# Optimization experiments

Measured on AMD Instinct MI355X. Metric: run time of the kernel, lower is better.

Reference implementation:

```python
import jax, jax.numpy as jnp
import numpy as np

D_MODEL = 1024
N_HEADS = 16
D_K = D_MODEL // N_HEADS
D_FF = 4096
B, S = 2, 2048
EPS = 1e-5
SCALE = 0.02


def setup_inputs() -> dict:
    key = jax.random.key(0)
    ks = jax.random.split(key, 8)
    return {
        "x": jax.random.normal(ks[0], (B, S, D_MODEL), dtype=jnp.float32),
        "ln1_w": jnp.ones((D_MODEL,), jnp.float32),
        "ln1_b": jnp.zeros((D_MODEL,), jnp.float32),
        "Wq": jax.random.normal(ks[1], (D_MODEL, D_MODEL), jnp.float32) * SCALE,
        "bq": jnp.zeros((D_MODEL,), jnp.float32),
        "Wk": jax.random.normal(ks[2], (D_MODEL, D_MODEL), jnp.float32) * SCALE,
        "bk": jnp.zeros((D_MODEL,), jnp.float32),
        "Wv": jax.random.normal(ks[3], (D_MODEL, D_MODEL), jnp.float32) * SCALE,
        "bv": jnp.zeros((D_MODEL,), jnp.float32),
        "Wo": jax.random.normal(ks[4], (D_MODEL, D_MODEL), jnp.float32) * SCALE,
        "bo": jnp.zeros((D_MODEL,), jnp.float32),
        "ln2_w": jnp.ones((D_MODEL,), jnp.float32),
        "ln2_b": jnp.zeros((D_MODEL,), jnp.float32),
        "W1": jax.random.normal(ks[5], (D_MODEL, D_FF), jnp.float32) * SCALE,
        "b1": jnp.zeros((D_FF,), jnp.float32),
        "W2": jax.random.normal(ks[6], (D_FF, D_MODEL), jnp.float32) * SCALE,
        "b2": jnp.zeros((D_MODEL,), jnp.float32),
    }


def _layernorm(x, w, b):
    mu = jnp.mean(x, axis=-1, keepdims=True)
    var = jnp.mean(jnp.square(x - mu), axis=-1, keepdims=True)
    return (x - mu) * jax.lax.rsqrt(var + EPS) * w + b


def reference(x, ln1_w, ln1_b, Wq, bq, Wk, bk, Wv, bv, Wo, bo,
              ln2_w, ln2_b, W1, b1, W2, b2):
    # Pre-norm multi-head self-attention (dropout = identity, eval mode)
    h = _layernorm(x, ln1_w, ln1_b)                      # [B,S,D]
    q = (h @ Wq + bq).reshape(B, S, N_HEADS, D_K)        # [B,S,H,Dk]
    k = (h @ Wk + bk).reshape(B, S, N_HEADS, D_K)
    v = (h @ Wv + bv).reshape(B, S, N_HEADS, D_K)
    scores = jnp.einsum('bqhd,bkhd->bhqk', q, k) / jnp.sqrt(jnp.float32(D_K))
    attn = jax.nn.softmax(scores, axis=-1)               # [B,H,S,S]
    ctx = jnp.einsum('bhqk,bkhd->bqhd', attn, v).reshape(B, S, D_MODEL)
    x = x + (ctx @ Wo + bo)
    # Pre-norm FFN
    h2 = _layernorm(x, ln2_w, ln2_b)
    ff = jax.nn.relu(h2 @ W1 + b1) @ W2 + b2
    return x + ff
```

## Files before the change

### kernel.cpp

```cpp
#include <hip/hip_runtime.h>
#include <hip/hip_bf16.h>
#include <cstdint>
#include <cstddef>

typedef unsigned short ushort_t;
typedef __bf16 bf16x8 __attribute__((ext_vector_type(8)));
typedef float f32x4 __attribute__((ext_vector_type(4)));
typedef float f32x16 __attribute__((ext_vector_type(16)));

#define D_MODEL 1024
#define D_FF 4096
#define BB 2
#define SS 2048
#define NH 16
#define MROWS (BB * SS)
#define KVBLK 64

__device__ __forceinline__ ushort_t f2bf(float f) {
  union { float f; unsigned u; } x; x.f = f;
  unsigned r = x.u + 0x7fffu + ((x.u >> 16) & 1u);
  return (ushort_t)(r >> 16);
}

__device__ __forceinline__ void gload_lds16(const void* g, void* l) {
  __builtin_amdgcn_global_load_lds((const __attribute__((address_space(1))) void*)g,
                                   (__attribute__((address_space(3))) void*)l, 16, 0, 0);
}

__device__ __forceinline__ bf16x8 pack4w(unsigned w0, unsigned w1, unsigned w2, unsigned w3) {
  union { unsigned u[4]; bf16x8 v; } t;
  t.u[0] = w0; t.u[1] = w1; t.u[2] = w2; t.u[3] = w3;
  return t.v;
}

__global__ __launch_bounds__(256) void ln_bf16_kernel(
    const float* __restrict__ x, const float* __restrict__ w,
    const float* __restrict__ b, ushort_t* __restrict__ out) {
  int row = blockIdx.x;
  int tid = threadIdx.x;
  int lane = tid & 63, wid = tid >> 6;
  const float4 v = ((const float4*)(x + (size_t)row * D_MODEL))[tid];
  float s = v.x + v.y + v.z + v.w;
  __shared__ float red[8];
  #pragma unroll
  for (int o = 32; o > 0; o >>= 1) s += __shfl_down(s, o);
  if (lane == 0) red[wid] = s;
  __syncthreads();
  float mu = (red[0] + red[1] + red[2] + red[3]) * (1.0f / D_MODEL);
  float d0 = v.x - mu, d1 = v.y - mu, d2 = v.z - mu, d3 = v.w - mu;
  float sq = d0 * d0 + d1 * d1 + d2 * d2 + d3 * d3;
  #pragma unroll
  for (int o = 32; o > 0; o >>= 1) sq += __shfl_down(sq, o);
  if (lane == 0) red[4 + wid] = sq;
  __syncthreads();
  float var = (red[4] + red[5] + red[6] + red[7]) * (1.0f / D_MODEL);
  float rstd = rsqrtf(var + 1e-5f);
  const float4 wv = ((const float4*)w)[tid];
  const float4 bv = ((const float4*)b)[tid];
  ushort4 o4;
  o4.x = f2bf(d0 * rstd * wv.x + bv.x);
  o4.y = f2bf(d1 * rstd * wv.y + bv.y);
  o4.z = f2bf(d2 * rstd * wv.z + bv.z);
  o4.w = f2bf(d3 * rstd * wv.w + bv.w);
  ((ushort4*)(out + (size_t)row * D_MODEL))[tid] = o4;
}

__global__ __launch_bounds__(256) void transpose_cast_kernel(
    const float* __restrict__ W, ushort_t* __restrict__ Wt, int K, int N) {
  __shared__ float tile[32][33];
  int bx = blockIdx.x * 32;
  int by = blockIdx.y * 32;
  int tx = threadIdx.x, ty = threadIdx.y;
  #pragma unroll
  for (int i = 0; i < 32; i += 8)
    tile[ty + i][tx] = W[(size_t)(by + ty + i) * N + bx + tx];
  __syncthreads();
  #pragma unroll
  for (int i = 0; i < 32; i += 8)
    Wt[(size_t)(bx + ty + i) * K + by + tx] = f2bf(tile[tx][ty + i]);
}

__global__ __launch_bounds__(256) void transpose_cast4_kernel(
    const float* __restrict__ Wq, const float* __restrict__ Wk,
    const float* __restrict__ Wv, const float* __restrict__ Wo,
    ushort_t* __restrict__ Dqkv, ushort_t* __restrict__ Do_) {
  __shared__ float tile[32][33];
  int z = blockIdx.z;
  const float* W = (z == 0) ? Wq : (z == 1) ? Wk : (z == 2) ? Wv : Wo;
  ushort_t* Wt = (z < 3) ? (Dqkv + (size_t)z * 1024 * 1024) : Do_;
  int bx = blockIdx.x * 32;
  int by = blockIdx.y * 32;
  int tx = threadIdx.x, ty = threadIdx.y;
  #pragma unroll
  for (int i = 0; i < 32; i += 8)
    tile[ty + i][tx] = W[(size_t)(by + ty + i) * 1024 + bx + tx];
  __syncthreads();
  #pragma unroll
  for (int i = 0; i < 32; i += 8)
    Wt[(size_t)(bx + ty + i) * 1024 + by + tx] = f2bf(tile[tx][ty + i]);
}

__global__ __launch_bounds__(256) void biaspack_kernel(
    const float* __restrict__ bq, const float* __restrict__ bk,
    const float* __restrict__ bv, float* __restrict__ out) {
  int i = blockIdx.x * 256 + threadIdx.x;
  float v = (i < 1024) ? bq[i] : (i < 2048) ? bk[i - 1024] : bv[i - 2048];
  out[i] = v;
}

__global__ __launch_bounds__(256) void vtrans_kernel(
    const ushort_t* __restrict__ qkv, ushort_t* __restrict__ Vt) {
  __shared__ __align__(16) ushort_t T[64 * 64];
  const int tid = threadIdx.x;
  const int bh = blockIdx.y, b = bh >> 4, h = bh & 15;
  const int kv0 = blockIdx.x * 64;
  const ushort_t* Vp = qkv + (size_t)b * SS * 3072 + 2048 + h * 64;
  #pragma unroll
  for (int i = 0; i < 2; i++) {
    int idx = tid * 2 + i;
    int key = idx >> 3, c = idx & 7;
    bf16x8 v = *(const bf16x8*)(Vp + (size_t)(kv0 + key) * 3072 + c * 8);
    *(bf16x8*)(T + key * 64 + ((c ^ (key & 7)) * 8)) = v;
  }
  __syncthreads();
  int d = tid >> 2, kb = tid & 3;
  ushort_t o[16];
  #pragma unroll
  for (int j = 0; j < 16; j++) {
    int key = kb * 16 + j;
    o[j] = T[key * 64 + (((d >> 3) ^ (key & 7)) * 8) + (d & 7)];
  }
  ushort_t* dst = Vt + (size_t)(bh * 64 + d) * SS + kv0 + kb * 16;
  *(bf16x8*)dst = *(bf16x8*)&o[0];
  *(bf16x8*)(dst + 8) = *(bf16x8*)&o[8];
}

template <int EPI>
__global__ __launch_bounds__(256, 2) void gemm256w_kernel(
    const ushort_t* __restrict__ A, const ushort_t* __restrict__ Bt,
    const float* __restrict__ bias, void* __restrict__ Cout,
    int M, int N, int K, int NTn) {
  __shared__ __align__(16) ushort_t ldsA[3][4096];
  __shared__ __align__(16) ushort_t ldsB[3][8192];
  const int tid = threadIdx.x, lane = tid & 63, wid = tid >> 6;
  const int wm = wid >> 1, wn = wid & 1;
  const int rl = lane & 15, cg = lane >> 4;
  int nwg = gridDim.x;
  int q = nwg >> 3, rr = nwg & 7;
  int xcd = blockIdx.x & 7, idx = blockIdx.x >> 3;
  int wgid = (xcd < rr ? xcd * (q + 1) : rr * (q + 1) + (xcd - rr) * q) + idx;
  const int row0 = (wgid / NTn) * 128, col0 = (wgid - (wgid / NTn) * NTn) * 256;
  const int NT = K / 32;

  int soffA[2], ldsoA[2], soffB[4], ldsoB[4];
  #pragma unroll
  for (int i = 0; i < 2; i++) {
    int ci = wid * 128 + i * 64 + lane;
    int P = ci * 16;
    int L = P ^ (((P >> 7) & 7) << 4);
    soffA[i] = (L >> 6) * K + ((L >> 4) & 3) * 8;
    ldsoA[i] = (wid * 128 + i * 64) * 8;
  }
  #pragma unroll
  for (int i = 0; i < 4; i++) {
    int ci = wid * 256 + i * 64 + lane;
    int P = ci * 16;
    int L = P ^ (((P >> 7) & 7) << 4);
    soffB[i] = (L >> 6) * K + ((L >> 4) & 3) * 8;
    ldsoB[i] = (wid * 256 + i * 64) * 8;
  }

  f32x4 acc[4][8] = {};

  auto stage = [&](int t, int b) {
    int kk = t * 32;
    #pragma unroll
    for (int i = 0; i < 2; i++)
      gload_lds16(A + (size_t)row0 * K + kk + soffA[i], &ldsA[b][ldsoA[i]]);
    #pragma unroll
    for (int i = 0; i < 4; i++)
      gload_lds16(Bt + (size_t)col0 * K + kk + soffB[i], &ldsB[b][ldsoB[i]]);
  };

  auto compute = [&](int b) {
    bf16x8 af[4], bfv[8];
    #pragma unroll
    for (int mi = 0; mi < 4; mi++) {
      int r = wm * 64 + mi * 16 + rl;
      int L = r * 64 + cg * 16;
      int P = L ^ (((L >> 7) & 7) << 4);
      af[mi] = *(const bf16x8*)&ldsA[b][P >> 1];
    }
    #pragma unroll
    for (int ni = 0; ni < 8; ni++) {
      int r = wn * 128 + ni * 16 + rl;
      int L = r * 64 + cg * 16;
      int P = L ^ (((L >> 7) & 7) << 4);
      bfv[ni] = *(const bf16x8*)&ldsB[b][P >> 1];
    }
    __builtin_amdgcn_s_setprio(1);
    #pragma unroll
    for (int mi = 0; mi < 4; mi++)
      #pragma unroll
      for (int ni = 0; ni < 8; ni++)
        acc[mi][ni] = __builtin_amdgcn_mfma_f32_16x16x32_bf16(af[mi], bfv[ni], acc[mi][ni], 0, 0, 0);
    __builtin_amdgcn_s_setprio(0);
  };

  stage(0, 0); stage(1, 1);
  int sb = 2, cb = 0;
  for (int t = 0; t < NT; ++t) {
    if (t < NT - 1) asm volatile("s_waitcnt vmcnt(6)" ::: "memory");
    else            asm volatile("s_waitcnt vmcnt(0)" ::: "memory");
    __builtin_amdgcn_s_barrier();
    __builtin_amdgcn_sched_barrier(0);
    if (t + 2 < NT) { stage(t + 2, sb); sb = (sb == 2) ? 0 : sb + 1; }
    compute(cb);
    cb = (cb == 2) ? 0 : cb + 1;
  }

  ushort_t* out = (ushort_t*)Cout;
  #pragma unroll
  for (int ni = 0; ni < 8; ni++) {
    int col = col0 + wn * 128 + ni * 16 + rl;
    float bv = bias[col];
    float sc = (EPI == 0 && col < 1024) ? 0.18033688011f : 1.0f;
    #pragma unroll
    for (int mi = 0; mi < 4; mi++) {
      int rowb = row0 + wm * 64 + mi * 16 + cg * 4;
      #pragma unroll
      for (int j = 0; j < 4; j++) {
        float v = acc[mi][ni][j] + bv;
        if (EPI == 1) v = fmaxf(v, 0.0f);
        if (EPI == 0) v *= sc;
        out[(size_t)(rowb + j) * N + col] = f2bf(v);
      }
    }
  }
}

template <int EPI>
__global__ __launch_bounds__(256, 3) void gemm128_kernel(
    const ushort_t* __restrict__ A, const ushort_t* __restrict__ Bt,
    const float* __restrict__ bias, const float* __restrict__ resid,
    void* __restrict__ Cout, int M, int N, int K, int NTn, int Ksplit, int MTN) {
  __shared__ __align__(16) ushort_t lds[3][2][4096];
  const int tid = threadIdx.x, lane = tid & 63, wid = tid >> 6;
  const int wm = wid >> 1, wn = wid & 1;
  const int rl = lane & 15, cg = lane >> 4;
  int nwg = gridDim.x;
  int q = nwg >> 3, rr = nwg & 7;
  int xcd = blockIdx.x & 7, idx = blockIdx.x >> 3;
  int wgid = (xcd < rr ? xcd * (q + 1) : rr * (q + 1) + (xcd - rr) * q) + idx;
  const int s = wgid / MTN;
  int rem = wgid - s * MTN;
  const int row0 = (rem / NTn) * 128, col0 = (rem - (rem / NTn) * NTn) * 128;
  const int k0 = s * Ksplit;
  const int NT = Ksplit / 32;

  int soff[2], ldso[2];
  #pragma unroll
  for (int i = 0; i < 2; i++) {
    int ci = wid * 128 + i * 64 + lane;
    int P = ci * 16;
    int L = P ^ (((P >> 7) & 7) << 4);
    int row = L >> 6, kc = (L >> 4) & 3;
    soff[i] = row * K + kc * 8;
    ldso[i] = (wid * 128 + i * 64) * 8;
  }

  f32x4 acc[4][4] = {};

  auto stage = [&](int t, int b) {
    int kk = k0 + t * 32;
    #pragma unroll
    for (int i = 0; i < 2; i++) {
      gload_lds16(A + (size_t)row0 * K + kk + soff[i], &lds[b][0][ldso[i]]);
      gload_lds16(Bt + (size_t)col0 * K + kk + soff[i], &lds[b][1][ldso[i]]);
    }
  };

  auto compute = [&](int b) {
    bf16x8 af[4], bfv[4];
    #pragma unroll
    for (int mi = 0; mi < 4; mi++) {
      int r = wm * 64 + mi * 16 + rl;
      int L = r * 64 + cg * 16;
      int P = L ^ (((L >> 7) & 7) << 4);
      af[mi] = *(const bf16x8*)&lds[b][0][P >> 1];
    }
    #pragma unroll
    for (int ni = 0; ni < 4; ni++) {
      int r = wn * 64 + ni * 16 + rl;
      int L = r * 64 + cg * 16;
      int P = L ^ (((L >> 7) & 7) << 4);
      bfv[ni] = *(const bf16x8*)&lds[b][1][P >> 1];
    }
    __builtin_amdgcn_s_setprio(1);
    #pragma unroll
    for (int mi = 0; mi < 4; mi++)
      #pragma unroll
      for (int ni = 0; ni < 4; ni++)
        acc[mi][ni] = __builtin_amdgcn_mfma_f32_16x16x32_bf16(af[mi], bfv[ni], acc[mi][ni], 0, 0, 0);
    __builtin_amdgcn_s_setprio(0);
  };

  stage(0, 0); stage(1, 1);
  int sb = 2, cb = 0;
  for (int t = 0; t < NT; ++t) {
    if (t < NT - 1) asm volatile("s_waitcnt vmcnt(4)" ::: "memory");
    else            asm volatile("s_waitcnt vmcnt(0)" ::: "memory");
    __builtin_amdgcn_s_barrier();
    __builtin_amdgcn_sched_barrier(0);
    if (t + 2 < NT) { stage(t + 2, sb); sb = (sb == 2) ? 0 : sb + 1; }
    compute(cb);
    cb = (cb == 2) ? 0 : cb + 1;
  }

  if (EPI == 2) {
    float* out = (float*)Cout;
    #pragma unroll
    for (int ni = 0; ni < 4; ni++) {
      int col = col0 + wn * 64 + ni * 16 + rl;
      float bv = bias[col];
      #pragma unroll
      for (int mi = 0; mi < 4; mi++) {
        int rowb = row0 + wm * 64 + mi * 16 + cg * 4;
        #pragma unroll
        for (int j = 0; j < 4; j++)
          out[(size_t)(rowb + j) * N + col] =
              acc[mi][ni][j] + bv + resid[(size_t)(rowb + j) * N + col];
      }
    }
  } else {
    float* out = (float*)Cout + (size_t)s * M * N;
    #pragma unroll
    for (int ni = 0; ni < 4; ni++) {
      int col = col0 + wn * 64 + ni * 16 + rl;
      #pragma unroll
      for (int mi = 0; mi < 4; mi++) {
        int rowb = row0 + wm * 64 + mi * 16 + cg * 4;
        #pragma unroll
        for (int j = 0; j < 4; j++)
          out[(size_t)(rowb + j) * N + col] = acc[mi][ni][j];
      }
    }
  }
}

__global__ __launch_bounds__(256) void reduce_kernel(
    const float* __restrict__ p, const float* __restrict__ bias,
    const float* __restrict__ resid, float* __restrict__ out,
    int S, size_t total4, size_t stride4) {
  const float4* p4 = (const float4*)p;
  const float4* r4 = (const float4*)resid;
  const float4* b4 = (const float4*)bias;
  float4* o4 = (float4*)out;
  for (size_t i = (size_t)blockIdx.x * 256 + threadIdx.x; i < total4;
       i += (size_t)gridDim.x * 256) {
    float4 a = r4[i];
    float4 bb = b4[i & 255];
    a.x += bb.x; a.y += bb.y; a.z += bb.z; a.w += bb.w;
    for (int s = 0; s < S; ++s) {
      float4 v = p4[(size_t)s * stride4 + i];
      a.x += v.x; a.y += v.y; a.z += v.z; a.w += v.w;
    }
    o4[i] = a;
  }
}

__global__ __launch_bounds__(256) void attn_kernel(
    const ushort_t* __restrict__ qkv, const ushort_t* __restrict__ Vt,
    ushort_t* __restrict__ ctx) {
  __shared__ __align__(16) ushort_t Kl[2][64 * 64];
  __shared__ __align__(16) ushort_t Vl[2][64 * 64];
  __shared__ float Lt[4][32];
  const int tid = threadIdx.x, lane = tid & 63, wid = tid >> 6;
  int bid = blockIdx.y * 16 + blockIdx.x;
  int w = (bid & 7) * 64 + (bid >> 3);
  const int bh = w >> 4, qt = w & 15;
  const int b = bh >> 4, h = bh & 15;
  const int q0w = qt * 128 + wid * 32;
  const int k31 = lane & 31, sg = lane >> 5, x7 = k31 & 7;
  const ushort_t* Qp = qkv + (size_t)b * SS * 3072 + h * 64;
  const ushort_t* Kp = Qp + 1024;
  const ushort_t* Vg = Vt + (size_t)bh * 64 * SS;

  bf16x8 qf[4];
  {
    const ushort_t* qb = Qp + (size_t)(q0w + k31) * 3072 + sg * 8;
    #pragma unroll
    for (int dsl = 0; dsl < 4; dsl++)
      qf[dsl] = *(const bf16x8*)(qb + dsl * 16);
  }
  float lsum = 0.f;
  f32x16 o0 = {}, o1 = {};

  const int NT = SS / KVBLK;

  int ksrc[2], vsrc[2];
  #pragma unroll
  for (int i = 0; i < 2; i++) {
    int idx = wid * 128 + i * 64 + lane;
    int R = idx >> 3, c = idx & 7;
    ksrc[i] = R * 3072 + ((c ^ (R & 7)) * 8);
    vsrc[i] = R * SS + ((c ^ (R & 7)) * 8);
  }
  const int ldsb = wid * 1024;

  auto stageKV = [&](int buf, int t) {
    size_t kvK = (size_t)t * KVBLK * 3072;
    int kvV = t * KVBLK;
    gload_lds16(Kp + kvK + ksrc[0], &Kl[buf][ldsb]);
    gload_lds16(Kp + kvK + ksrc[1], &Kl[buf][ldsb + 512]);
    gload_lds16(Vg + kvV + vsrc[0], &Vl[buf][ldsb]);
    gload_lds16(Vg + kvV + vsrc[1], &Vl[buf][ldsb + 512]);
  };

  auto softmax_half = [&](const f32x16& s, bf16x8& paE, bf16x8& paO) {
    float pv[16];
    #pragma unroll
    for (int r = 0; r < 16; r++) pv[r] = __builtin_amdgcn_exp2f(s[r]);
    #pragma unroll
    for (int r = 0; r < 16; r++) lsum += pv[r];
    unsigned W[4][2];
    #pragma unroll
    for (int qd = 0; qd < 4; qd++) {
      asm("v_cvt_pk_bf16_f32 %0, %1, %2" : "=v"(W[qd][0]) : "v"(pv[4 * qd]), "v"(pv[4 * qd + 1]));
      asm("v_cvt_pk_bf16_f32 %0, %1, %2" : "=v"(W[qd][1]) : "v"(pv[4 * qd + 2]), "v"(pv[4 * qd + 3]));
    }
    unsigned a0 = W[1][0], b0 = W[0][0], a1 = W[1][1], b1 = W[0][1];
    asm("v_permlane32_swap_b32 %0, %1" : "+v"(a0), "+v"(b0));
    asm("v_permlane32_swap_b32 %0, %1" : "+v"(a1), "+v"(b1));
    paE = pack4w(b0, b1, a0, a1);
    unsigned a2 = W[3][0], b2 = W[2][0], a3 = W[3][1], b3 = W[2][1];
    asm("v_permlane32_swap_b32 %0, %1" : "+v"(a2), "+v"(b2));
    asm("v_permlane32_swap_b32 %0, %1" : "+v"(a3), "+v"(b3));
    paO = pack4w(b2, b3, a2, a3);
  };

  auto body = [&](int t, int cb) {
    __syncthreads();
    if (t + 1 < NT) stageKV(cb ^ 1, t + 1);

    f32x16 s0 = {}, s1 = {};
    #pragma unroll
    for (int dsl = 0; dsl < 4; dsl++) {
      int ch = ((dsl * 2 + sg) ^ x7) * 8;
      bf16x8 kf0 = *(const bf16x8*)(&Kl[cb][k31 * 64 + ch]);
      bf16x8 kf1 = *(const bf16x8*)(&Kl[cb][(32 + k31) * 64 + ch]);
      s0 = __builtin_amdgcn_mfma_f32_32x32x16_bf16(kf0, qf[dsl], s0, 0, 0, 0);
      s1 = __builtin_amdgcn_mfma_f32_32x32x16_bf16(kf1, qf[dsl], s1, 0, 0, 0);
    }
    bf16x8 pa[4];
    softmax_half(s0, pa[0], pa[1]);
    softmax_half(s1, pa[2], pa[3]);
    #pragma unroll
    for (int ks = 0; ks < 4; ks++) {
      int ch = ((2 * ks + sg) ^ x7) * 8;
      bf16x8 vf0 = *(const bf16x8*)(&Vl[cb][k31 * 64 + ch]);
      bf16x8 vf1 = *(const bf16x8*)(&Vl[cb][(32 + k31) * 64 + ch]);
      o0 = __builtin_amdgcn_mfma_f32_32x32x16_bf16(pa[ks], vf0, o0, 0, 0, 0);
      o1 = __builtin_amdgcn_mfma_f32_32x32x16_bf16(pa[ks], vf1, o1, 0, 0, 0);
    }
  };

  stageKV(0, 0);
  for (int t = 0; t < NT; t += 2) {
    body(t, 0);
    body(t + 1, 1);
  }

  float ltot = lsum + __shfl_xor(lsum, 32);
  if (lane < 32) Lt[wid][lane] = ltot;
  asm volatile("s_waitcnt lgkmcnt(0)" ::: "memory");
  __builtin_amdgcn_sched_barrier(0);

  const int colb = h * 64 + k31;
  #pragma unroll
  for (int r = 0; r < 16; r++) {
    int qp = (r & 3) + 8 * (r >> 2) + 4 * sg;
    float rlq = 1.0f / Lt[wid][qp];
    size_t row = (size_t)(b * SS + q0w + qp);
    ctx[row * D_MODEL + colb] = f2bf(o0[r] * rlq);
    ctx[row * D_MODEL + colb + 32] = f2bf(o1[r] * rlq);
  }
}

extern "C" void kernel_launch(void* const* d_in, const int* in_sizes, int n_in,
                              void* d_out, int out_size, void* d_ws, size_t ws_size,
                              hipStream_t stream) {
  const float* x    = (const float*)d_in[0];
  const float* ln1w = (const float*)d_in[1];
  const float* ln1b = (const float*)d_in[2];
  const float* Wq   = (const float*)d_in[3];
  const float* bq   = (const float*)d_in[4];
  const float* Wk   = (const float*)d_in[5];
  const float* bk   = (const float*)d_in[6];
  const float* Wv   = (const float*)d_in[7];
  const float* bv   = (const float*)d_in[8];
  const float* Wo   = (const float*)d_in[9];
  const float* bo   = (const float*)d_in[10];
  const float* ln2w = (const float*)d_in[11];
  const float* ln2b = (const float*)d_in[12];
  const float* W1   = (const float*)d_in[13];
  const float* b1   = (const float*)d_in[14];
  const float* W2   = (const float*)d_in[15];
  const float* b2   = (const float*)d_in[16];

  char* ws = (char*)d_ws;
  size_t off = 0;
  auto alloc = [&](size_t bytes) {
    void* p = ws + off;
    off += (bytes + 255) & ~(size_t)255;
    return p;
  };
  ushort_t* Wt_qkv = (ushort_t*)alloc((size_t)3072 * 1024 * 2);
  ushort_t* Wt_o   = (ushort_t*)alloc((size_t)1024 * 1024 * 2);
  ushort_t* Wt_1   = (ushort_t*)alloc((size_t)4096 * 1024 * 2);
  ushort_t* Wt_2   = (ushort_t*)alloc((size_t)1024 * 4096 * 2);
  float*    bqkv   = (float*)alloc((size_t)3072 * 4);
  ushort_t* qkvb   = (ushort_t*)alloc((size_t)MROWS * 3072 * 2);
  ushort_t* ctxb   = (ushort_t*)alloc((size_t)MROWS * 1024 * 2);
  ushort_t* hbuf   = (ushort_t*)alloc((size_t)MROWS * 1024 * 2);
  float*    x2     = (float*)alloc((size_t)MROWS * 1024 * 4);
  ushort_t* Vtb    = (ushort_t*)alloc((size_t)BB * NH * 64 * SS * 2);
  ushort_t* ff1    = qkvb;
  float*    outp   = (float*)d_out;

  const size_t partial1 = (size_t)MROWS * 1024 * 4;
  int S = (ws_size - off >= 2 * partial1 + 256) ? 2 : 1;
  float* pbuf = (S == 2) ? (float*)alloc(2 * partial1) : nullptr;

  dim3 tb(32, 8);
  transpose_cast4_kernel<<<dim3(32, 32, 4), tb, 0, stream>>>(Wq, Wk, Wv, Wo, Wt_qkv, Wt_o);
  transpose_cast_kernel<<<dim3(128, 32), tb, 0, stream>>>(W1, Wt_1, 1024, 4096);
  transpose_cast_kernel<<<dim3(32, 128), tb, 0, stream>>>(W2, Wt_2, 4096, 1024);
  biaspack_kernel<<<12, 256, 0, stream>>>(bq, bk, bv, bqkv);

  ln_bf16_kernel<<<MROWS, 256, 0, stream>>>(x, ln1w, ln1b, hbuf);
  gemm256w_kernel<0><<<dim3(32 * 12), 256, 0, stream>>>(
      hbuf, Wt_qkv, bqkv, qkvb, MROWS, 3072, 1024, 12);
  vtrans_kernel<<<dim3(SS / 64, BB * NH), 256, 0, stream>>>(qkvb, Vtb);
  attn_kernel<<<dim3(SS / 128, BB * NH), 256, 0, stream>>>(qkvb, Vtb, ctxb);
  gemm128_kernel<2><<<dim3(8 * 32), 256, 0, stream>>>(
      ctxb, Wt_o, bo, x, x2, MROWS, 1024, 1024, 8, 1024, 8 * 32);
  ln_bf16_kernel<<<MROWS, 256, 0, stream>>>(x2, ln2w, ln2b, hbuf);
  gemm256w_kernel<1><<<dim3(32 * 16), 256, 0, stream>>>(
      hbuf, Wt_1, b1, ff1, MROWS, D_FF, 1024, 16);
  if (S == 2) {
    gemm128_kernel<3><<<dim3(8 * 32 * 2), 256, 0, stream>>>(
        ff1, Wt_2, nullptr, nullptr, pbuf, MROWS, 1024, 4096, 8, 2048, 8 * 32);
    reduce_kernel<<<2048, 256, 0, stream>>>(pbuf, b2, x2, outp, 2,
        (size_t)MROWS * 1024 / 4, (size_t)MROWS * 1024 / 4);
  } else {
    gemm128_kernel<2><<<dim3(8 * 32), 256, 0, stream>>>(
        ff1, Wt_2, b2, x2, outp, MROWS, 1024, 4096, 8, 4096, 8 * 32);
  }
}
```

Before: 232.2 us.

## Triple-buffer attention K/V tiles with explicit vmcnt waits and split accumulators

The attention kernel moves from double- to triple-buffered K/V LDS tiles. It prefetches two tiles ahead and uses explicit s_waitcnt vmcnt plus a raw s_barrier instead of __syncthreads, so global loads stay in flight across iterations. The PV accumulators are split into four chains to shorten MFMA dependency chains, and the row-sum reduction becomes a tree. The cost is more LDS, which may lower occupancy, and extra accumulator registers.

```diff
diff --git a/kernel.cpp b/kernel.cpp
--- a/kernel.cpp
+++ b/kernel.cpp
@@ -372,8 +372,8 @@
 __global__ __launch_bounds__(256) void attn_kernel(
     const ushort_t* __restrict__ qkv, const ushort_t* __restrict__ Vt,
     ushort_t* __restrict__ ctx) {
-  __shared__ __align__(16) ushort_t Kl[2][64 * 64];
-  __shared__ __align__(16) ushort_t Vl[2][64 * 64];
+  __shared__ __align__(16) ushort_t Kl[3][64 * 64];
+  __shared__ __align__(16) ushort_t Vl[3][64 * 64];
   __shared__ float Lt[4][32];
   const int tid = threadIdx.x, lane = tid & 63, wid = tid >> 6;
   int bid = blockIdx.y * 16 + blockIdx.x;
@@ -394,7 +394,7 @@
       qf[dsl] = *(const bf16x8*)(qb + dsl * 16);
   }
   float lsum = 0.f;
-  f32x16 o0 = {}, o1 = {};
+  f32x16 oA = {}, oB = {}, oC = {}, oD = {};
 
   const int NT = SS / KVBLK;
 
@@ -421,28 +421,27 @@
     float pv[16];
     #pragma unroll
     for (int r = 0; r < 16; r++) pv[r] = __builtin_amdgcn_exp2f(s[r]);
-    #pragma unroll
-    for (int r = 0; r < 16; r++) lsum += pv[r];
+    float a0 = pv[0] + pv[1], a1 = pv[2] + pv[3], a2 = pv[4] + pv[5], a3 = pv[6] + pv[7];
+    float a4 = pv[8] + pv[9], a5 = pv[10] + pv[11], a6 = pv[12] + pv[13], a7 = pv[14] + pv[15];
+    float b0 = a0 + a1, b1 = a2 + a3, b2 = a4 + a5, b3 = a6 + a7;
+    lsum += (b0 + b1) + (b2 + b3);
     unsigned W[4][2];
     #pragma unroll
     for (int qd = 0; qd < 4; qd++) {
       asm("v_cvt_pk_bf16_f32 %0, %1, %2" : "=v"(W[qd][0]) : "v"(pv[4 * qd]), "v"(pv[4 * qd + 1]));
       asm("v_cvt_pk_bf16_f32 %0, %1, %2" : "=v"(W[qd][1]) : "v"(pv[4 * qd + 2]), "v"(pv[4 * qd + 3]));
     }
-    unsigned a0 = W[1][0], b0 = W[0][0], a1 = W[1][1], b1 = W[0][1];
-    asm("v_permlane32_swap_b32 %0, %1" : "+v"(a0), "+v"(b0));
-    asm("v_permlane32_swap_b32 %0, %1" : "+v"(a1), "+v"(b1));
-    paE = pack4w(b0, b1, a0, a1);
-    unsigned a2 = W[3][0], b2 = W[2][0], a3 = W[3][1], b3 = W[2][1];
-    asm("v_permlane32_swap_b32 %0, %1" : "+v"(a2), "+v"(b2));
-    asm("v_permlane32_swap_b32 %0, %1" : "+v"(a3), "+v"(b3));
-    paO = pack4w(b2, b3, a2, a3);
+    unsigned a0w = W[1][0], b0w = W[0][0], a1w = W[1][1], b1w = W[0][1];
+    asm("v_permlane32_swap_b32 %0, %1" : "+v"(a0w), "+v"(b0w));
+    asm("v_permlane32_swap_b32 %0, %1" : "+v"(a1w), "+v"(b1w));
+    paE = pack4w(b0w, b1w, a0w, a1w);
+    unsigned a2w = W[3][0], b2w = W[2][0], a3w = W[3][1], b3w = W[2][1];
+    asm("v_permlane32_swap_b32 %0, %1" : "+v"(a2w), "+v"(b2w));
+    asm("v_permlane32_swap_b32 %0, %1" : "+v"(a3w), "+v"(b3w));
+    paO = pack4w(b2w, b3w, a2w, a3w);
   };
 
   auto body = [&](int t, int cb) {
-    __syncthreads();
-    if (t + 1 < NT) stageKV(cb ^ 1, t + 1);
-
     f32x16 s0 = {}, s1 = {};
     #pragma unroll
     for (int dsl = 0; dsl < 4; dsl++) {
@@ -460,15 +459,27 @@
       int ch = ((2 * ks + sg) ^ x7) * 8;
       bf16x8 vf0 = *(const bf16x8*)(&Vl[cb][k31 * 64 + ch]);
       bf16x8 vf1 = *(const bf16x8*)(&Vl[cb][(32 + k31) * 64 + ch]);
-      o0 = __builtin_amdgcn_mfma_f32_32x32x16_bf16(pa[ks], vf0, o0, 0, 0, 0);
-      o1 = __builtin_amdgcn_mfma_f32_32x32x16_bf16(pa[ks], vf1, o1, 0, 0, 0);
+      if (ks < 2) {
+        oA = __builtin_amdgcn_mfma_f32_32x32x16_bf16(pa[ks], vf0, oA, 0, 0, 0);
+        oC = __builtin_amdgcn_mfma_f32_32x32x16_bf16(pa[ks], vf1, oC, 0, 0, 0);
+      } else {
+        oB = __builtin_amdgcn_mfma_f32_32x32x16_bf16(pa[ks], vf0, oB, 0, 0, 0);
+        oD = __builtin_amdgcn_mfma_f32_32x32x16_bf16(pa[ks], vf1, oD, 0, 0, 0);
+      }
     }
   };
 
   stageKV(0, 0);
-  for (int t = 0; t < NT; t += 2) {
-    body(t, 0);
-    body(t + 1, 1);
+  stageKV(1, 1);
+  int sb = 2, cb = 0;
+  for (int t = 0; t < NT; ++t) {
+    if (t < NT - 1) asm volatile("s_waitcnt vmcnt(4)" ::: "memory");
+    else            asm volatile("s_waitcnt vmcnt(0)" ::: "memory");
+    __builtin_amdgcn_s_barrier();
+    __builtin_amdgcn_sched_barrier(0);
+    if (t + 2 < NT) { stageKV(sb, t + 2); sb = (sb == 2) ? 0 : sb + 1; }
+    body(t, cb);
+    cb = (cb == 2) ? 0 : cb + 1;
   }
 
   float ltot = lsum + __shfl_xor(lsum, 32);
@@ -476,6 +487,7 @@
   asm volatile("s_waitcnt lgkmcnt(0)" ::: "memory");
   __builtin_amdgcn_sched_barrier(0);
 
+  f32x16 o0 = oA + oB, o1 = oC + oD;
   const int colb = h * 64 + k31;
   #pragma unroll
   for (int r = 0; r < 16; r++) {
```

After: 238.1 us. 1.03x slower.

## Split attention over two KV halves and combine partial outputs in a new kernel

Applied to the files above, without the earlier changes.

The attention kernel now runs a third grid dimension of two splits, each processing half of the key/value sequence. Each split writes unnormalised fp32 partial outputs and row sums to workspace. A new combine kernel adds the two halves, normalises and casts to bf16. The goal is to double the number of blocks so more CUs are busy, at the cost of extra fp32 global traffic and one more launch. Combining by simply adding the sums is only valid if the softmax applies no per-split running max. The FFN2 split-K path is also made unconditional by always allocating the partial buffer.

```diff
diff --git a/kernel.cpp b/kernel.cpp
--- a/kernel.cpp
+++ b/kernel.cpp
@@ -371,11 +371,11 @@
 
 __global__ __launch_bounds__(256) void attn_kernel(
     const ushort_t* __restrict__ qkv, const ushort_t* __restrict__ Vt,
-    ushort_t* __restrict__ ctx) {
+    float* __restrict__ Op, float* __restrict__ Lp) {
   __shared__ __align__(16) ushort_t Kl[2][64 * 64];
   __shared__ __align__(16) ushort_t Vl[2][64 * 64];
-  __shared__ float Lt[4][32];
   const int tid = threadIdx.x, lane = tid & 63, wid = tid >> 6;
+  const int split = blockIdx.z;
   int bid = blockIdx.y * 16 + blockIdx.x;
   int w = (bid & 7) * 64 + (bid >> 3);
   const int bh = w >> 4, qt = w & 15;
@@ -383,8 +383,8 @@
   const int q0w = qt * 128 + wid * 32;
   const int k31 = lane & 31, sg = lane >> 5, x7 = k31 & 7;
   const ushort_t* Qp = qkv + (size_t)b * SS * 3072 + h * 64;
-  const ushort_t* Kp = Qp + 1024;
-  const ushort_t* Vg = Vt + (size_t)bh * 64 * SS;
+  const ushort_t* Kp = Qp + 1024 + (size_t)split * 1024 * 3072;
+  const ushort_t* Vg = Vt + (size_t)bh * 64 * SS + split * 1024;
 
   bf16x8 qf[4];
   {
@@ -396,7 +396,7 @@
   float lsum = 0.f;
   f32x16 o0 = {}, o1 = {};
 
-  const int NT = SS / KVBLK;
+  const int NT = 1024 / KVBLK;
 
   int ksrc[2], vsrc[2];
   #pragma unroll
@@ -472,19 +472,38 @@
   }
 
   float ltot = lsum + __shfl_xor(lsum, 32);
-  if (lane < 32) Lt[wid][lane] = ltot;
-  asm volatile("s_waitcnt lgkmcnt(0)" ::: "memory");
-  __builtin_amdgcn_sched_barrier(0);
-
+  if (lane < 32)
+    Lp[(size_t)split * 32 * SS + bh * SS + q0w + lane] = ltot;
+
+  float* Ob = Op + (size_t)split * MROWS * 1024;
   const int colb = h * 64 + k31;
   #pragma unroll
   for (int r = 0; r < 16; r++) {
     int qp = (r & 3) + 8 * (r >> 2) + 4 * sg;
-    float rlq = 1.0f / Lt[wid][qp];
     size_t row = (size_t)(b * SS + q0w + qp);
-    ctx[row * D_MODEL + colb] = f2bf(o0[r] * rlq);
-    ctx[row * D_MODEL + colb + 32] = f2bf(o1[r] * rlq);
-  }
+    Ob[row * 1024 + colb] = o0[r];
+    Ob[row * 1024 + colb + 32] = o1[r];
+  }
+}
+
+__global__ __launch_bounds__(256) void attn_combine_kernel(
+    const float* __restrict__ Op, const float* __restrict__ Lp,
+    ushort_t* __restrict__ ctx) {
+  int row = blockIdx.x;
+  int tid = threadIdx.x;
+  int col = tid * 4;
+  int b = row >> 11, q = row & 2047;
+  int bh = b * 16 + (col >> 6);
+  float l = Lp[bh * SS + q] + Lp[32 * SS + bh * SS + q];
+  float rl = 1.0f / l;
+  const float4 a = *(const float4*)(Op + (size_t)row * 1024 + col);
+  const float4 c = *(const float4*)(Op + (size_t)MROWS * 1024 + (size_t)row * 1024 + col);
+  ushort4 o;
+  o.x = f2bf((a.x + c.x) * rl);
+  o.y = f2bf((a.y + c.y) * rl);
+  o.z = f2bf((a.z + c.z) * rl);
+  o.w = f2bf((a.w + c.w) * rl);
+  *(ushort4*)(ctx + (size_t)row * D_MODEL + col) = o;
 }
 
 extern "C" void kernel_launch(void* const* d_in, const int* in_sizes, int n_in,
@@ -529,8 +548,9 @@
   float*    outp   = (float*)d_out;
 
   const size_t partial1 = (size_t)MROWS * 1024 * 4;
-  int S = (ws_size - off >= 2 * partial1 + 256) ? 2 : 1;
-  float* pbuf = (S == 2) ? (float*)alloc(2 * partial1) : nullptr;
+  float* obuf = (float*)alloc(2 * partial1);
+  float* lbuf = (float*)alloc((size_t)2 * 32 * SS * 4);
+  float* pbuf = obuf;
 
   dim3 tb(32, 8);
   transpose_cast4_kernel<<<dim3(32, 32, 4), tb, 0, stream>>>(Wq, Wk, Wv, Wo, Wt_qkv, Wt_o);
@@ -542,19 +562,15 @@
   gemm256w_kernel<0><<<dim3(32 * 12), 256, 0, stream>>>(
       hbuf, Wt_qkv, bqkv, qkvb, MROWS, 3072, 1024, 12);
   vtrans_kernel<<<dim3(SS / 64, BB * NH), 256, 0, stream>>>(qkvb, Vtb);
-  attn_kernel<<<dim3(SS / 128, BB * NH), 256, 0, stream>>>(qkvb, Vtb, ctxb);
+  attn_kernel<<<dim3(SS / 128, BB * NH, 2), 256, 0, stream>>>(qkvb, Vtb, obuf, lbuf);
+  attn_combine_kernel<<<MROWS, 256, 0, stream>>>(obuf, lbuf, ctxb);
   gemm128_kernel<2><<<dim3(8 * 32), 256, 0, stream>>>(
       ctxb, Wt_o, bo, x, x2, MROWS, 1024, 1024, 8, 1024, 8 * 32);
   ln_bf16_kernel<<<MROWS, 256, 0, stream>>>(x2, ln2w, ln2b, hbuf);
   gemm256w_kernel<1><<<dim3(32 * 16), 256, 0, stream>>>(
       hbuf, Wt_1, b1, ff1, MROWS, D_FF, 1024, 16);
-  if (S == 2) {
-    gemm128_kernel<3><<<dim3(8 * 32 * 2), 256, 0, stream>>>(
-        ff1, Wt_2, nullptr, nullptr, pbuf, MROWS, 1024, 4096, 8, 2048, 8 * 32);
-    reduce_kernel<<<2048, 256, 0, stream>>>(pbuf, b2, x2, outp, 2,
-        (size_t)MROWS * 1024 / 4, (size_t)MROWS * 1024 / 4);
-  } else {
-    gemm128_kernel<2><<<dim3(8 * 32), 256, 0, stream>>>(
-        ff1, Wt_2, b2, x2, outp, MROWS, 1024, 4096, 8, 4096, 8 * 32);
-  }
-}
+  gemm128_kernel<3><<<dim3(8 * 32 * 2), 256, 0, stream>>>(
+      ff1, Wt_2, nullptr, nullptr, pbuf, MROWS, 1024, 4096, 8, 2048, 8 * 32);
+  reduce_kernel<<<2048, 256, 0, stream>>>(pbuf, b2, x2, outp, 2,
+      (size_t)MROWS * 1024 / 4, (size_t)MROWS * 1024 / 4);
+}
```

Result: slower. 241.4 us (+4.0%).
